# Optimization experiments

Hardware: AMD Instinct MI355X
Metric: run time of the kernel (lower is better)

## Reference

```python
import jax, jax.numpy as jnp
import numpy as np
import math

B, T, D = 2, 2048, 1024
H = 16
DH = D // H
DFF = 4096
EPS = 1e-5


def setup_inputs() -> dict:
    key = jax.random.key(0)
    ks = jax.random.split(key, 10)
    x = jax.random.normal(ks[0], (B, T, D), dtype=jnp.float32)
    # bool mask, True above diagonal => masked (matches masked_fill semantics)
    causal_mask = jnp.triu(jnp.ones((T, T), dtype=bool), k=1)
    s = 0.02
    return {
        "x": x,
        "causal_mask": causal_mask,
        "gamma1": jnp.ones((D,), jnp.float32),
        "beta1": jnp.zeros((D,), jnp.float32),
        "wq": jax.random.normal(ks[1], (D, D), jnp.float32) * s,
        "wk": jax.random.normal(ks[2], (D, D), jnp.float32) * s,
        "wv": jax.random.normal(ks[3], (D, D), jnp.float32) * s,
        "wo": jax.random.normal(ks[4], (D, D), jnp.float32) * s,
        "gamma2": jnp.ones((D,), jnp.float32),
        "beta2": jnp.zeros((D,), jnp.float32),
        "w1": jax.random.normal(ks[5], (D, DFF), jnp.float32) * s,
        "b1": jnp.zeros((DFF,), jnp.float32),
        "w2": jax.random.normal(ks[6], (DFF, D), jnp.float32) * s,
        "b2": jnp.zeros((D,), jnp.float32),
    }


def _layer_norm(x, gamma, beta):
    mean = jnp.mean(x, axis=-1, keepdims=True)
    var = jnp.mean((x - mean) ** 2, axis=-1, keepdims=True)
    xhat = (x - mean) / jnp.sqrt(var + EPS)
    return gamma * xhat + beta


def _split_heads(x):
    b, t, d = x.shape
    return x.reshape(b, t, H, DH).transpose(0, 2, 1, 3)  # (B,H,T,Dh)


def reference(x, causal_mask, gamma1, beta1, wq, wk, wv, wo,
              gamma2, beta2, w1, b1, w2, b2):
    # --- attention sublayer (pre-LN) ---
    h = _layer_norm(x, gamma1, beta1)
    q = _split_heads(h @ wq)
    k = _split_heads(h @ wk)
    v = _split_heads(h @ wv)
    scores = jnp.einsum('bhqd,bhkd->bhqk', q, k) / math.sqrt(DH)  # (B,H,T,T)
    scores = jnp.where(causal_mask[None, None, :, :], -jnp.inf, scores)
    attn = jax.nn.softmax(scores, axis=-1)
    out = jnp.einsum('bhqk,bhkd->bhqd', attn, v)
    out = out.transpose(0, 2, 1, 3).reshape(x.shape)  # merge heads
    attn_out = out @ wo
    x = x + attn_out
    # --- FFN sublayer (pre-LN) ---
    h = _layer_norm(x, gamma2, beta2)
    ffn = jax.nn.gelu(h @ w1 + b1, approximate=False) @ w2 + b2
    return x + ffn
```

## Files before the change

kernel.cpp:

```cpp
#include <hip/hip_runtime.h>
#include <hip/hip_bf16.h>
#include <math.h>

#define B_   2
#define T_   2048
#define D_   1024
#define H_   16
#define DH_  64
#define DFF_ 4096
#define NTOK (B_*T_)

typedef __attribute__((ext_vector_type(8))) short short8;
typedef __attribute__((ext_vector_type(4))) float f32x4;

static __device__ __forceinline__ short f2bf(float f) {
    union { __hip_bfloat16 h; short s; } u;
    u.h = __float2bfloat16(f);
    return u.s;
}

static __device__ __forceinline__ f32x4 mfma16(short8 a, short8 b, f32x4 c) {
    return __builtin_amdgcn_mfma_f32_16x16x32_bf16(a, b, c, 0, 0, 0);
}

static __device__ __forceinline__ void gload16(const void* g, void* l) {
    __builtin_amdgcn_global_load_lds(
        (__attribute__((address_space(1))) void*)g,
        (__attribute__((address_space(3))) void*)l, 16, 0, 0);
}

static __device__ __forceinline__ short8 lds_read_sw(const short* base, int row, int kbyte) {
    const int off = (row << 7) + (kbyte ^ ((row & 7) << 4));
    return *reinterpret_cast<const short8*>(reinterpret_cast<const char*>(base) + off);
}

static __device__ __forceinline__ void tc_body(
    const float* __restrict__ src, short* __restrict__ dst,
    int K, int N, float scale, int bx, int by, int t)
{
    __shared__ short tile[64][68];
    const int k0 = by * 64, n0 = bx * 64;
    #pragma unroll
    for (int j = 0; j < 4; ++j) {
        const int i = j * 256 + t;
        const int k = i >> 4, c = i & 15;
        const float4 v = *reinterpret_cast<const float4*>(
            src + (size_t)(k0 + k) * N + n0 + c * 4);
        short4 s4;
        s4.x = f2bf(v.x * scale);
        s4.y = f2bf(v.y * scale);
        s4.z = f2bf(v.z * scale);
        s4.w = f2bf(v.w * scale);
        *reinterpret_cast<short4*>(&tile[k][c * 4]) = s4;
    }
    __syncthreads();
    #pragma unroll
    for (int j = 0; j < 4; ++j) {
        const int i = j * 256 + t;
        const int n = i >> 4, c = i & 15;
        short4 s4;
        s4.x = tile[c * 4 + 0][n];
        s4.y = tile[c * 4 + 1][n];
        s4.z = tile[c * 4 + 2][n];
        s4.w = tile[c * 4 + 3][n];
        *reinterpret_cast<short4*>(dst + (size_t)(n0 + n) * K + k0 + c * 4) = s4;
    }
}

__global__ __launch_bounds__(256) void transpose_cast4(
    const float* __restrict__ s0, const float* __restrict__ s1,
    const float* __restrict__ s2, const float* __restrict__ s3,
    short* __restrict__ d0, short* __restrict__ d1,
    short* __restrict__ d2, short* __restrict__ d3, float scale0)
{
    const int z = blockIdx.z;
    const float* src = (z == 0) ? s0 : (z == 1) ? s1 : (z == 2) ? s2 : s3;
    short*       dst = (z == 0) ? d0 : (z == 1) ? d1 : (z == 2) ? d2 : d3;
    const float scale = (z == 0) ? scale0 : 1.0f;
    tc_body(src, dst, 1024, 1024, scale, blockIdx.x, blockIdx.y, threadIdx.x);
}

__global__ __launch_bounds__(256) void transpose_cast_ffn(
    const float* __restrict__ w1, short* __restrict__ w1T,
    const float* __restrict__ w2, short* __restrict__ w2T)
{
    int bid = blockIdx.x;
    if (bid < 1024) {
        tc_body(w1, w1T, 1024, 4096, 1.0f, bid & 63, bid >> 6, threadIdx.x);
    } else {
        bid -= 1024;
        tc_body(w2, w2T, 4096, 1024, 1.0f, bid & 15, bid >> 4, threadIdx.x);
    }
}

__global__ __launch_bounds__(256) void ln_kernel(
    const float* __restrict__ in, const float* __restrict__ gamma,
    const float* __restrict__ beta, short* __restrict__ out)
{
    const int row = blockIdx.x * 4 + (threadIdx.x >> 6);
    const int l = threadIdx.x & 63;
    const float* rp = in + (size_t)row * D_;
    float4 v[4];
    float s = 0.f, sq = 0.f;
    #pragma unroll
    for (int j = 0; j < 4; ++j) {
        v[j] = *reinterpret_cast<const float4*>(rp + j * 256 + l * 4);
        s  += v[j].x + v[j].y + v[j].z + v[j].w;
        sq += v[j].x*v[j].x + v[j].y*v[j].y + v[j].z*v[j].z + v[j].w*v[j].w;
    }
    #pragma unroll
    for (int off = 32; off >= 1; off >>= 1) {
        s  += __shfl_xor(s, off);
        sq += __shfl_xor(sq, off);
    }
    const float mean = s * (1.0f / D_);
    float var = sq * (1.0f / D_) - mean * mean;
    var = fmaxf(var, 0.0f);
    const float rstd = rsqrtf(var + 1e-5f);
    #pragma unroll
    for (int j = 0; j < 4; ++j) {
        const float4 g = *reinterpret_cast<const float4*>(gamma + j * 256 + l * 4);
        const float4 b = *reinterpret_cast<const float4*>(beta  + j * 256 + l * 4);
        short4 o;
        o.x = f2bf(g.x * ((v[j].x - mean) * rstd) + b.x);
        o.y = f2bf(g.y * ((v[j].y - mean) * rstd) + b.y);
        o.z = f2bf(g.z * ((v[j].z - mean) * rstd) + b.z);
        o.w = f2bf(g.w * ((v[j].w - mean) * rstd) + b.w);
        *reinterpret_cast<short4*>(out + (size_t)row * D_ + j * 256 + l * 4) = o;
    }
}

template<int BM, int BN, int EPI>
__global__ __launch_bounds__(512) void gemm_kernel(
    const short* __restrict__ A, const short* __restrict__ Bt,
    void* __restrict__ Cout, const float* __restrict__ resid,
    const float* __restrict__ bias, short* __restrict__ vaux,
    int M, int N, int K, int nbx)
{
    constexpr int MB = BM / 4 / 16;
    constexpr int NB = BN / 2 / 16;
    constexpr int JA = BM / 64;
    constexpr int JB = BN / 64;
    constexpr int J  = JA + JB;
    __shared__ short As[2][BM * 64];
    __shared__ short Bs[2][BN * 64];
    const int t = threadIdx.x;
    const int wid = t >> 6, lane = t & 63;
    const int lr = lane & 15, lk = lane >> 4;
    const int cpx = (int)gridDim.x >> 3;
    const int bid = (int)blockIdx.x;
    const int swz = (bid & 7) * cpx + (bid >> 3);
    const int m0 = (swz / nbx) * BM, n0 = (swz % nbx) * BN;
    const int wrow = (wid >> 1) * (BM / 4);
    const int wcol = (wid & 1) * (BN / 2);

    const char* aSrc[JA];
    const char* bSrc[JB];
    #pragma unroll
    for (int j = 0; j < JA; ++j) {
        const int off = j * 8192 + t * 16;
        const int r   = off >> 7;
        const int cb  = (off & 127) ^ ((r & 7) << 4);
        aSrc[j] = (const char*)(A + (size_t)(m0 + r) * K) + cb;
    }
    #pragma unroll
    for (int j = 0; j < JB; ++j) {
        const int off = j * 8192 + t * 16;
        const int r   = off >> 7;
        const int cb  = (off & 127) ^ ((r & 7) << 4);
        bSrc[j] = (const char*)(Bt + (size_t)(n0 + r) * K) + cb;
    }

    f32x4 acc[MB][NB];
    #pragma unroll
    for (int m = 0; m < MB; ++m)
        #pragma unroll
        for (int n = 0; n < NB; ++n) acc[m][n] = (f32x4){0.f, 0.f, 0.f, 0.f};

    const int NT = K >> 6;

    auto stage = [&](int bufsel, int ktile) {
        const int kb = ktile << 7;
        #pragma unroll
        for (int j = 0; j < JA; ++j)
            gload16(aSrc[j] + kb, (char*)As[bufsel] + j * 8192 + wid * 1024);
        #pragma unroll
        for (int j = 0; j < JB; ++j)
            gload16(bSrc[j] + kb, (char*)Bs[bufsel] + j * 8192 + wid * 1024);
    };
    auto compute = [&](int bufsel) {
        #pragma unroll
        for (int kk = 0; kk < 64; kk += 32) {
            short8 af[MB], bf[NB];
            #pragma unroll
            for (int m = 0; m < MB; ++m)
                af[m] = lds_read_sw(As[bufsel], wrow + m * 16 + lr, (kk + lk * 8) * 2);
            #pragma unroll
            for (int n = 0; n < NB; ++n)
                bf[n] = lds_read_sw(Bs[bufsel], wcol + n * 16 + lr, (kk + lk * 8) * 2);
            #pragma unroll
            for (int m = 0; m < MB; ++m)
                #pragma unroll
                for (int n = 0; n < NB; ++n)
                    acc[m][n] = mfma16(af[m], bf[n], acc[m][n]);
        }
    };

    stage(0, 0);
    stage(1, 1);

    for (int kt = 0; kt < NT - 1; ++kt) {
        asm volatile("s_waitcnt vmcnt(%0)" :: "n"(J) : "memory");
        __builtin_amdgcn_s_barrier();
        compute(kt & 1);
        __builtin_amdgcn_s_barrier();
        if (kt + 2 < NT) stage(kt & 1, kt + 2);
    }
    asm volatile("s_waitcnt vmcnt(0)" ::: "memory");
    __builtin_amdgcn_s_barrier();
    compute((NT - 1) & 1);

    #pragma unroll
    for (int m = 0; m < MB; ++m) {
        #pragma unroll
        for (int n = 0; n < NB; ++n) {
            #pragma unroll
            for (int r = 0; r < 4; ++r) {
                const int gr = m0 + wrow + m * 16 + lk * 4 + r;
                const int gc = n0 + wcol + n * 16 + lr;
                const size_t idx = (size_t)gr * N + gc;
                const float v = acc[m][n][r];
                if constexpr (EPI == 1) {
                    ((float*)Cout)[idx] = resid[idx] + v;
                } else if constexpr (EPI == 3) {
                    ((float*)Cout)[idx] = resid[idx] + v + bias[gc];
                } else {
                    if (gc < 2048) {
                        ((short*)Cout)[idx] = f2bf(v);
                    } else {
                        const int hh = (gc - 2048) >> 6, dh = (gc - 2048) & 63;
                        const int bb = gr >> 11, tl = gr & 2047;
                        vaux[((size_t)((bb << 4) + hh) * 64 + dh) * 2048 + tl] = f2bf(v);
                    }
                }
            }
        }
    }
}

__global__ __launch_bounds__(512) void gemm256_kernel(
    const short* __restrict__ A, const short* __restrict__ Bt,
    short* __restrict__ Cout, const float* __restrict__ bias,
    int K, int N, int nbx)
{
    __shared__ short As[2][16384];
    __shared__ short Bs[2][16384];
    const int t = threadIdx.x;
    const int wid = t >> 6, lane = t & 63;
    const int lr = lane & 15, lk = lane >> 4;
    const int cpx = (int)gridDim.x >> 3;
    const int bid = (int)blockIdx.x;
    const int swz = (bid & 7) * cpx + (bid >> 3);
    const int m0 = (swz / nbx) * 256, n0 = (swz % nbx) * 256;
    const int wr = (wid >> 2) * 128;
    const int wc = (wid & 3) * 64;

    const char* aSrc[4];
    const char* bSrc[4];
    #pragma unroll
    for (int j = 0; j < 4; ++j) {
        const int off = j * 8192 + t * 16;
        const int r   = off >> 7;
        const int cb  = (off & 127) ^ ((r & 7) << 4);
        aSrc[j] = (const char*)(A  + (size_t)(m0 + r) * K) + cb;
        bSrc[j] = (const char*)(Bt + (size_t)(n0 + r) * K) + cb;
    }

    f32x4 acc[8][4];
    #pragma unroll
    for (int m = 0; m < 8; ++m)
        #pragma unroll
        for (int n = 0; n < 4; ++n) acc[m][n] = (f32x4){0.f, 0.f, 0.f, 0.f};

    const int NT = K >> 6;

    auto stageA = [&](int d, int ktile) {
        const int kb = ktile << 7;
        #pragma unroll
        for (int j = 0; j < 4; ++j)
            gload16(aSrc[j] + kb, (char*)As[d] + j * 8192 + wid * 1024);
    };
    auto stageB = [&](int d, int ktile) {
        const int kb = ktile << 7;
        #pragma unroll
        for (int j = 0; j < 4; ++j)
            gload16(bSrc[j] + kb, (char*)Bs[d] + j * 8192 + wid * 1024);
    };

    stageA(0, 0); stageB(0, 0);
    stageB(1, 1); stageA(1, 1);

    for (int kt = 0; kt < NT - 1; ++kt) {
        const int d = kt & 1;
        asm volatile("s_waitcnt vmcnt(8)" ::: "memory");
        __builtin_amdgcn_s_barrier();
        short8 bf[4][2];
        #pragma unroll
        for (int n = 0; n < 4; ++n)
            #pragma unroll
            for (int q = 0; q < 2; ++q)
                bf[n][q] = lds_read_sw(Bs[d], wc + n * 16 + lr, (q * 32 + lk * 8) * 2);
        {
            short8 af[2][2];
            #pragma unroll
            for (int m = 0; m < 2; ++m)
                #pragma unroll
                for (int q = 0; q < 2; ++q)
                    af[m][q] = lds_read_sw(As[d], wr + m * 16 + lr, (q * 32 + lk * 8) * 2);
            asm volatile("s_waitcnt lgkmcnt(0)" ::: "memory");
            __builtin_amdgcn_s_setprio(1);
            #pragma unroll
            for (int m = 0; m < 2; ++m)
                #pragma unroll
                for (int n = 0; n < 4; ++n)
                    #pragma unroll
                    for (int q = 0; q < 2; ++q)
                        acc[m][n] = mfma16(af[m][q], bf[n][q], acc[m][n]);
            __builtin_amdgcn_s_setprio(0);
        }
        __builtin_amdgcn_s_barrier();
        if (kt + 2 < NT) stageB(d, kt + 2);
        #pragma unroll
        for (int p = 1; p < 4; ++p) {
            short8 af[2][2];
            #pragma unroll
            for (int m = 0; m < 2; ++m)
                #pragma unroll
                for (int q = 0; q < 2; ++q)
                    af[m][q] = lds_read_sw(As[d], wr + (p * 2 + m) * 16 + lr, (q * 32 + lk * 8) * 2);
            asm volatile("s_waitcnt lgkmcnt(0)" ::: "memory");
            __builtin_amdgcn_s_setprio(1);
            #pragma unroll
            for (int m = 0; m < 2; ++m)
                #pragma unroll
                for (int n = 0; n < 4; ++n)
                    #pragma unroll
                    for (int q = 0; q < 2; ++q)
                        acc[p * 2 + m][n] = mfma16(af[m][q], bf[n][q], acc[p * 2 + m][n]);
            __builtin_amdgcn_s_setprio(0);
        }
        __builtin_amdgcn_s_barrier();
        if (kt + 2 < NT) stageA(d, kt + 2);
    }
    {
        const int d = (NT - 1) & 1;
        asm volatile("s_waitcnt vmcnt(0)" ::: "memory");
        __builtin_amdgcn_s_barrier();
        short8 bf[4][2];
        #pragma unroll
        for (int n = 0; n < 4; ++n)
            #pragma unroll
            for (int q = 0; q < 2; ++q)
                bf[n][q] = lds_read_sw(Bs[d], wc + n * 16 + lr, (q * 32 + lk * 8) * 2);
        #pragma unroll
        for (int p = 0; p < 4; ++p) {
            short8 af[2][2];
            #pragma unroll
            for (int m = 0; m < 2; ++m)
                #pragma unroll
                for (int q = 0; q < 2; ++q)
                    af[m][q] = lds_read_sw(As[d], wr + (p * 2 + m) * 16 + lr, (q * 32 + lk * 8) * 2);
            asm volatile("s_waitcnt lgkmcnt(0)" ::: "memory");
            __builtin_amdgcn_s_setprio(1);
            #pragma unroll
            for (int m = 0; m < 2; ++m)
                #pragma unroll
                for (int n = 0; n < 4; ++n)
                    #pragma unroll
                    for (int q = 0; q < 2; ++q)
                        acc[p * 2 + m][n] = mfma16(af[m][q], bf[n][q], acc[p * 2 + m][n]);
            __builtin_amdgcn_s_setprio(0);
        }
    }

    #pragma unroll
    for (int m = 0; m < 8; ++m) {
        #pragma unroll
        for (int n = 0; n < 4; ++n) {
            #pragma unroll
            for (int r = 0; r < 4; ++r) {
                const int gr = m0 + wr + m * 16 + lk * 4 + r;
                const int gc = n0 + wc + n * 16 + lr;
                const float tt = acc[m][n][r] + bias[gc];
                const float z  = 2.3025851f * (tt + 0.044715f * tt * tt * tt);
                const float e2 = __builtin_amdgcn_exp2f(-z);
                const float ge = tt * __builtin_amdgcn_rcpf(1.0f + e2);
                Cout[(size_t)gr * N + gc] = f2bf(ge);
            }
        }
    }
}

static __device__ __forceinline__ void attn_tile(
    const short* Kcur, const short* Vcur, char* pw,
    short8 qf0, short8 qf1, int q0, int kvb, bool diag,
    int lr, int lk, f32x4 (&o)[4], float (&ls)[4])
{
    f32x4 s[4];
    #pragma unroll
    for (int n = 0; n < 4; ++n) s[n] = (f32x4){0.f, 0.f, 0.f, 0.f};
    #pragma unroll
    for (int n = 0; n < 4; ++n) {
        s[n] = mfma16(qf0, lds_read_sw(Kcur, n * 16 + lr, (lk * 8) * 2), s[n]);
        s[n] = mfma16(qf1, lds_read_sw(Kcur, n * 16 + lr, (32 + lk * 8) * 2), s[n]);
    }
    #pragma unroll
    for (int r = 0; r < 4; ++r) {
        const int qg = q0 + lk * 4 + r;
        float v0 = s[0][r], v1 = s[1][r], v2 = s[2][r], v3 = s[3][r];
        if (diag) {
            if (kvb +      lr > qg) v0 = -INFINITY;
            if (kvb + 16 + lr > qg) v1 = -INFINITY;
            if (kvb + 32 + lr > qg) v2 = -INFINITY;
            if (kvb + 48 + lr > qg) v3 = -INFINITY;
        }
        const float p0 = __builtin_amdgcn_exp2f(v0);
        const float p1 = __builtin_amdgcn_exp2f(v1);
        const float p2 = __builtin_amdgcn_exp2f(v2);
        const float p3 = __builtin_amdgcn_exp2f(v3);
        ls[r] += p0 + p1 + p2 + p3;
        const int prow = lk * 4 + r;
        const int sw = (prow & 7) << 4;
        char* prb = pw + prow * 128;
        *(short*)(prb + (((     lr * 2)) ^ sw)) = f2bf(p0);
        *(short*)(prb + ((32 + lr * 2) ^ sw)) = f2bf(p1);
        *(short*)(prb + ((64 + lr * 2) ^ sw)) = f2bf(p2);
        *(short*)(prb + ((96 + lr * 2) ^ sw)) = f2bf(p3);
    }
    asm volatile("s_waitcnt lgkmcnt(0)" ::: "memory");
    #pragma unroll
    for (int kk = 0; kk < 2; ++kk) {
        const short8 pf = *reinterpret_cast<const short8*>(
            pw + lr * 128 + ((kk * 64 + lk * 16) ^ ((lr & 7) << 4)));
        #pragma unroll
        for (int n = 0; n < 4; ++n)
            o[n] = mfma16(pf, lds_read_sw((const short*)Vcur, n * 16 + lr, (kk * 32 + lk * 8) * 2), o[n]);
    }
}

__global__ __launch_bounds__(256) void attn_kernel(
    const short* __restrict__ qkv, const short* __restrict__ vT,
    short* __restrict__ attn)
{
    __shared__ short Ks[2][4096];
    __shared__ short Vs[2][4096];
    __shared__ short Ps[2][4][1024];
    const int xx = blockIdx.x;
    const int bh = blockIdx.y;
    const int qA = xx, qB = 31 - xx;
    const int b = bh >> 4, h = bh & 15;
    const int t = threadIdx.x;
    const int wid = t >> 6, lane = t & 63;
    const int lr = lane & 15, lk = lane >> 4;
    const int q0A = qA * 64 + wid * 16;
    const int q0B = qB * 64 + wid * 16;

    const short* qrowA = qkv + (size_t)(b * T_ + q0A + lr) * 3072 + h * 64;
    const short8 qfA0 = *reinterpret_cast<const short8*>(qrowA + lk * 8);
    const short8 qfA1 = *reinterpret_cast<const short8*>(qrowA + 32 + lk * 8);
    const short* qrowB = qkv + (size_t)(b * T_ + q0B + lr) * 3072 + h * 64;
    const short8 qfB0 = *reinterpret_cast<const short8*>(qrowB + lk * 8);
    const short8 qfB1 = *reinterpret_cast<const short8*>(qrowB + 32 + lk * 8);
    const short* kbase = qkv + (size_t)b * T_ * 3072 + 1024 + h * 64;
    const short* vbase = vT + (size_t)bh * 64 * T_;

    f32x4 oA[4], oB[4];
    float lsA[4], lsB[4];
    #pragma unroll
    for (int n = 0; n < 4; ++n) {
        oA[n] = (f32x4){0.f, 0.f, 0.f, 0.f};
        oB[n] = (f32x4){0.f, 0.f, 0.f, 0.f};
    }
    #pragma unroll
    for (int r = 0; r < 4; ++r) { lsA[r] = 0.f; lsB[r] = 0.f; }

    const int nkt = qB + 1;

    #pragma unroll
    for (int j = 0; j < 2; ++j) {
        const int off = j * 4096 + t * 16;
        const int r   = off >> 7;
        const int cb  = (off & 127) ^ ((r & 7) << 4);
        gload16(kbase + (size_t)r * 3072 + (cb >> 1), (char*)Ks[0] + j * 4096 + wid * 1024);
        gload16(vbase + (size_t)r * T_   + (cb >> 1), (char*)Vs[0] + j * 4096 + wid * 1024);
    }
    __syncthreads();

    int cur = 0;
    for (int kt = 0; kt < nkt; ++kt) {
        const int kvb = kt * 64;
        if (kt + 1 < nkt) {
            const int nb = kvb + 64;
            #pragma unroll
            for (int j = 0; j < 2; ++j) {
                const int off = j * 4096 + t * 16;
                const int r   = off >> 7;
                const int cb  = (off & 127) ^ ((r & 7) << 4);
                gload16(kbase + (size_t)(nb + r) * 3072 + (cb >> 1),
                        (char*)Ks[cur ^ 1] + j * 4096 + wid * 1024);
                gload16(vbase + (size_t)r * T_ + nb + (cb >> 1),
                        (char*)Vs[cur ^ 1] + j * 4096 + wid * 1024);
            }
        }

        attn_tile(Ks[cur], Vs[cur], (char*)&Ps[1][wid][0],
                  qfB0, qfB1, q0B, kvb, kt == qB, lr, lk, oB, lsB);
        if (kt <= qA)
            attn_tile(Ks[cur], Vs[cur], (char*)&Ps[0][wid][0],
                      qfA0, qfA1, q0A, kvb, kt == qA, lr, lk, oA, lsA);

        __syncthreads();
        cur ^= 1;
    }

    #pragma unroll
    for (int r = 0; r < 4; ++r) {
        float lA = lsA[r], lB = lsB[r];
        lA += __shfl_xor(lA, 1); lB += __shfl_xor(lB, 1);
        lA += __shfl_xor(lA, 2); lB += __shfl_xor(lB, 2);
        lA += __shfl_xor(lA, 4); lB += __shfl_xor(lB, 4);
        lA += __shfl_xor(lA, 8); lB += __shfl_xor(lB, 8);
        const float invA = 1.0f / lA, invB = 1.0f / lB;
        short* opA = attn + (size_t)(b * T_ + q0A + lk * 4 + r) * D_ + h * 64;
        short* opB = attn + (size_t)(b * T_ + q0B + lk * 4 + r) * D_ + h * 64;
        #pragma unroll
        for (int n = 0; n < 4; ++n) {
            opA[n * 16 + lr] = f2bf(oA[n][r] * invA);
            opB[n * 16 + lr] = f2bf(oB[n][r] * invB);
        }
    }
}

extern "C" void kernel_launch(void* const* d_in, const int* in_sizes, int n_in,
                              void* d_out, int out_size, void* d_ws, size_t ws_size,
                              hipStream_t stream)
{
    (void)in_sizes; (void)n_in; (void)out_size; (void)ws_size;
    const float* x      = (const float*)d_in[0];
    const float* gamma1 = (const float*)d_in[2];
    const float* beta1  = (const float*)d_in[3];
    const float* wq     = (const float*)d_in[4];
    const float* wk     = (const float*)d_in[5];
    const float* wv     = (const float*)d_in[6];
    const float* wo     = (const float*)d_in[7];
    const float* gamma2 = (const float*)d_in[8];
    const float* beta2  = (const float*)d_in[9];
    const float* w1     = (const float*)d_in[10];
    const float* b1     = (const float*)d_in[11];
    const float* w2     = (const float*)d_in[12];
    const float* b2     = (const float*)d_in[13];
    float* out = (float*)d_out;

    char* ws = (char*)d_ws;
    size_t off = 0;
    short* wqkvT = (short*)(ws + off); off += (size_t)3072 * 1024 * 2;
    short* woT   = (short*)(ws + off); off += (size_t)1024 * 1024 * 2;
    short* w1T   = (short*)(ws + off); off += (size_t)4096 * 1024 * 2;
    short* w2T   = (short*)(ws + off); off += (size_t)1024 * 4096 * 2;
    short* h1    = (short*)(ws + off); off += (size_t)NTOK * 1024 * 2;
    short* h2    = (short*)(ws + off); off += (size_t)NTOK * 1024 * 2;
    float* y     = (float*)(ws + off); off += (size_t)NTOK * 1024 * 4;
    short* attnb = (short*)(ws + off); off += (size_t)NTOK * 1024 * 2;
    short* qkv   = (short*)(ws + off); off += (size_t)NTOK * 3072 * 2;
    short* vT    = (short*)(ws + off); off += (size_t)B_ * H_ * DH_ * T_ * 2;
    short* g     = qkv;

    transpose_cast4<<<dim3(16, 16, 4), 256, 0, stream>>>(
        wq, wk, wv, wo,
        wqkvT, wqkvT + 1024 * 1024, wqkvT + 2048 * 1024, woT,
        0.18033688011112042f);
    transpose_cast_ffn<<<2048, 256, 0, stream>>>(w1, w1T, w2, w2T);

    ln_kernel<<<NTOK / 4, 256, 0, stream>>>(x, gamma1, beta1, h1);

    gemm_kernel<128, 128, 4><<<768, 512, 0, stream>>>(
        h1, wqkvT, qkv, nullptr, nullptr, vT, NTOK, 3072, 1024, 24);

    attn_kernel<<<dim3(16, 32), 256, 0, stream>>>(qkv, vT, attnb);

    gemm_kernel<128, 64, 1><<<512, 512, 0, stream>>>(
        attnb, woT, y, x, nullptr, nullptr, NTOK, 1024, 1024, 16);

    ln_kernel<<<NTOK / 4, 256, 0, stream>>>(y, gamma2, beta2, h2);

    gemm256_kernel<<<256, 512, 0, stream>>>(h2, w1T, g, b1, 1024, 4096, 16);

    gemm_kernel<128, 64, 3><<<512, 512, 0, stream>>>(
        g, w2T, out, y, b2, nullptr, NTOK, 1024, 4096, 16);
}
```

Before: 228.1 us.

## Fuse weight prep with first LayerNorm and double KV tiles per attention stage

```diff
diff --git a/kernel.cpp b/kernel.cpp
--- a/kernel.cpp
+++ b/kernel.cpp
@@ -67,38 +67,13 @@
     }
 }
 
-__global__ __launch_bounds__(256) void transpose_cast4(
-    const float* __restrict__ s0, const float* __restrict__ s1,
-    const float* __restrict__ s2, const float* __restrict__ s3,
-    short* __restrict__ d0, short* __restrict__ d1,
-    short* __restrict__ d2, short* __restrict__ d3, float scale0)
-{
-    const int z = blockIdx.z;
-    const float* src = (z == 0) ? s0 : (z == 1) ? s1 : (z == 2) ? s2 : s3;
-    short*       dst = (z == 0) ? d0 : (z == 1) ? d1 : (z == 2) ? d2 : d3;
-    const float scale = (z == 0) ? scale0 : 1.0f;
-    tc_body(src, dst, 1024, 1024, scale, blockIdx.x, blockIdx.y, threadIdx.x);
-}
-
-__global__ __launch_bounds__(256) void transpose_cast_ffn(
-    const float* __restrict__ w1, short* __restrict__ w1T,
-    const float* __restrict__ w2, short* __restrict__ w2T)
-{
-    int bid = blockIdx.x;
-    if (bid < 1024) {
-        tc_body(w1, w1T, 1024, 4096, 1.0f, bid & 63, bid >> 6, threadIdx.x);
-    } else {
-        bid -= 1024;
-        tc_body(w2, w2T, 4096, 1024, 1.0f, bid & 15, bid >> 4, threadIdx.x);
-    }
-}
-
-__global__ __launch_bounds__(256) void ln_kernel(
+static __device__ __forceinline__ void ln_body(
     const float* __restrict__ in, const float* __restrict__ gamma,
-    const float* __restrict__ beta, short* __restrict__ out)
-{
-    const int row = blockIdx.x * 4 + (threadIdx.x >> 6);
-    const int l = threadIdx.x & 63;
+    const float* __restrict__ beta, short* __restrict__ out,
+    int rowblk, int t)
+{
+    const int row = rowblk * 4 + (t >> 6);
+    const int l = t & 63;
     const float* rp = in + (size_t)row * D_;
     float4 v[4];
     float s = 0.f, sq = 0.f;
@@ -127,6 +102,43 @@
         o.z = f2bf(g.z * ((v[j].z - mean) * rstd) + b.z);
         o.w = f2bf(g.w * ((v[j].w - mean) * rstd) + b.w);
         *reinterpret_cast<short4*>(out + (size_t)row * D_ + j * 256 + l * 4) = o;
+    }
+}
+
+__global__ __launch_bounds__(256) void ln_kernel(
+    const float* __restrict__ in, const float* __restrict__ gamma,
+    const float* __restrict__ beta, short* __restrict__ out)
+{
+    ln_body(in, gamma, beta, out, blockIdx.x, threadIdx.x);
+}
+
+__global__ __launch_bounds__(256) void prep_kernel(
+    const float* __restrict__ wq, const float* __restrict__ wk,
+    const float* __restrict__ wv, const float* __restrict__ wo,
+    short* __restrict__ wqkvT, short* __restrict__ woT,
+    const float* __restrict__ w1, short* __restrict__ w1T,
+    const float* __restrict__ w2, short* __restrict__ w2T,
+    const float* __restrict__ x, const float* __restrict__ gamma1,
+    const float* __restrict__ beta1, short* __restrict__ h1, float qscale)
+{
+    const int bid = blockIdx.x;
+    const int t = threadIdx.x;
+    if (bid < 1024) {
+        const int z = bid >> 8, r8 = bid & 255;
+        const float* src = (z == 0) ? wq : (z == 1) ? wk : (z == 2) ? wv : wo;
+        short* dst = (z == 3) ? woT : (wqkvT + (size_t)z * 1024 * 1024);
+        const float scale = (z == 0) ? qscale : 1.0f;
+        tc_body(src, dst, 1024, 1024, scale, r8 & 15, r8 >> 4, t);
+    } else if (bid < 3072) {
+        int b2 = bid - 1024;
+        if (b2 < 1024) {
+            tc_body(w1, w1T, 1024, 4096, 1.0f, b2 & 63, b2 >> 6, t);
+        } else {
+            b2 -= 1024;
+            tc_body(w2, w2T, 4096, 1024, 1.0f, b2 & 15, b2 >> 4, t);
+        }
+    } else {
+        ln_body(x, gamma1, beta1, h1, bid - 3072, t);
     }
 }
 
@@ -452,8 +464,8 @@
     const short* __restrict__ qkv, const short* __restrict__ vT,
     short* __restrict__ attn)
 {
-    __shared__ short Ks[2][4096];
-    __shared__ short Vs[2][4096];
+    __shared__ short Ks[2][2][4096];
+    __shared__ short Vs[2][2][4096];
     __shared__ short Ps[2][4][1024];
     const int xx = blockIdx.x;
     const int bh = blockIdx.y;
@@ -485,39 +497,55 @@
     for (int r = 0; r < 4; ++r) { lsA[r] = 0.f; lsB[r] = 0.f; }
 
     const int nkt = qB + 1;
-
-    #pragma unroll
-    for (int j = 0; j < 2; ++j) {
-        const int off = j * 4096 + t * 16;
-        const int r   = off >> 7;
-        const int cb  = (off & 127) ^ ((r & 7) << 4);
-        gload16(kbase + (size_t)r * 3072 + (cb >> 1), (char*)Ks[0] + j * 4096 + wid * 1024);
-        gload16(vbase + (size_t)r * T_   + (cb >> 1), (char*)Vs[0] + j * 4096 + wid * 1024);
+    const int nst = (nkt + 1) >> 1;
+
+    #pragma unroll
+    for (int ss = 0; ss < 2; ++ss) {
+        const int kv0 = ss * 64;
+        #pragma unroll
+        for (int j = 0; j < 2; ++j) {
+            const int off = j * 4096 + t * 16;
+            const int r   = off >> 7;
+            const int cb  = (off & 127) ^ ((r & 7) << 4);
+            gload16(kbase + (size_t)(kv0 + r) * 3072 + (cb >> 1),
+                    (char*)Ks[0][ss] + j * 4096 + wid * 1024);
+            gload16(vbase + (size_t)r * T_ + kv0 + (cb >> 1),
+                    (char*)Vs[0][ss] + j * 4096 + wid * 1024);
+        }
     }
     __syncthreads();
 
     int cur = 0;
-    for (int kt = 0; kt < nkt; ++kt) {
-        const int kvb = kt * 64;
-        if (kt + 1 < nkt) {
-            const int nb = kvb + 64;
-            #pragma unroll
-            for (int j = 0; j < 2; ++j) {
-                const int off = j * 4096 + t * 16;
-                const int r   = off >> 7;
-                const int cb  = (off & 127) ^ ((r & 7) << 4);
-                gload16(kbase + (size_t)(nb + r) * 3072 + (cb >> 1),
-                        (char*)Ks[cur ^ 1] + j * 4096 + wid * 1024);
-                gload16(vbase + (size_t)r * T_ + nb + (cb >> 1),
-                        (char*)Vs[cur ^ 1] + j * 4096 + wid * 1024);
+    for (int st = 0; st < nst; ++st) {
+        if (st + 1 < nst) {
+            const int nb = (st + 1) * 128;
+            #pragma unroll
+            for (int ss = 0; ss < 2; ++ss) {
+                const int kv0 = nb + ss * 64;
+                #pragma unroll
+                for (int j = 0; j < 2; ++j) {
+                    const int off = j * 4096 + t * 16;
+                    const int r   = off >> 7;
+                    const int cb  = (off & 127) ^ ((r & 7) << 4);
+                    gload16(kbase + (size_t)(kv0 + r) * 3072 + (cb >> 1),
+                            (char*)Ks[cur ^ 1][ss] + j * 4096 + wid * 1024);
+                    gload16(vbase + (size_t)r * T_ + kv0 + (cb >> 1),
+                            (char*)Vs[cur ^ 1][ss] + j * 4096 + wid * 1024);
+                }
             }
         }
 
-        attn_tile(Ks[cur], Vs[cur], (char*)&Ps[1][wid][0],
-                  qfB0, qfB1, q0B, kvb, kt == qB, lr, lk, oB, lsB);
-        if (kt <= qA)
-            attn_tile(Ks[cur], Vs[cur], (char*)&Ps[0][wid][0],
-                      qfA0, qfA1, q0A, kvb, kt == qA, lr, lk, oA, lsA);
+        #pragma unroll
+        for (int ss = 0; ss < 2; ++ss) {
+            const int kt = st * 2 + ss;
+            const int kvb = kt * 64;
+            if (kt <= qB)
+                attn_tile(Ks[cur][ss], Vs[cur][ss], (char*)&Ps[1][wid][0],
+                          qfB0, qfB1, q0B, kvb, kt == qB, lr, lk, oB, lsB);
+            if (kt <= qA)
+                attn_tile(Ks[cur][ss], Vs[cur][ss], (char*)&Ps[0][wid][0],
+                          qfA0, qfA1, q0A, kvb, kt == qA, lr, lk, oA, lsA);
+        }
 
         __syncthreads();
         cur ^= 1;
@@ -575,13 +603,9 @@
     short* vT    = (short*)(ws + off); off += (size_t)B_ * H_ * DH_ * T_ * 2;
     short* g     = qkv;
 
-    transpose_cast4<<<dim3(16, 16, 4), 256, 0, stream>>>(
-        wq, wk, wv, wo,
-        wqkvT, wqkvT + 1024 * 1024, wqkvT + 2048 * 1024, woT,
-        0.18033688011112042f);
-    transpose_cast_ffn<<<2048, 256, 0, stream>>>(w1, w1T, w2, w2T);
-
-    ln_kernel<<<NTOK / 4, 256, 0, stream>>>(x, gamma1, beta1, h1);
+    prep_kernel<<<4096, 256, 0, stream>>>(
+        wq, wk, wv, wo, wqkvT, woT, w1, w1T, w2, w2T,
+        x, gamma1, beta1, h1, 0.18033688011112042f);
 
     gemm_kernel<128, 128, 4><<<768, 512, 0, stream>>>(
         h1, wqkvT, qkv, nullptr, nullptr, vT, NTOK, 3072, 1024, 24);
```

New measurement: 228.3 us. Within noise of the previous version (+0.1%).
